# Kernel tuning notes

Hardware: AMD Instinct MI355X
Metric: run time of the kernel (lower is better)

Reference implementation:

```python
import jax, jax.numpy as jnp
import numpy as np

S, B, E, H, Q, T, K, N = 256, 32, 768, 1024, 64, 512, 11, 16
STD = 2.5
EPS = 1e-5


def gaussian_kernel(size, std):
    t = np.linspace(-(size - 1) / 2, (size - 1) / 2, size)
    x, y = np.meshgrid(t, t)
    kern = np.exp(-0.5 * (x ** 2 + y ** 2) / std ** 2)
    return (kern / kern.sum()).astype(np.float32)


def setup_inputs() -> dict:
    key = jax.random.key(0)
    ks = jax.random.split(key, 24)
    s = 0.05
    inp = {
        'sentence_batch': jax.random.normal(ks[0], (S, B, E), jnp.float32),
        # forward LSTM params (torch layout: W_ih (4H,E), W_hh (4H,H), gate order i,f,g,o)
        'Wih_f': jax.random.normal(ks[1], (4 * H, E), jnp.float32) * s,
        'Whh_f': jax.random.normal(ks[2], (4 * H, H), jnp.float32) * s,
        'bih_f': jnp.zeros((4 * H,), jnp.float32),
        'bhh_f': jnp.zeros((4 * H,), jnp.float32),
        # backward LSTM params
        'Wih_b': jax.random.normal(ks[3], (4 * H, E), jnp.float32) * s,
        'Whh_b': jax.random.normal(ks[4], (4 * H, H), jnp.float32) * s,
        'bih_b': jnp.zeros((4 * H,), jnp.float32),
        'bhh_b': jnp.zeros((4 * H,), jnp.float32),
        # layer norms
        'g_in': jnp.ones((E,), jnp.float32), 'be_in': jnp.zeros((E,), jnp.float32),
        'g_fw': jnp.ones((H,), jnp.float32), 'be_fw': jnp.zeros((H,), jnp.float32),
        'g_bk': jnp.ones((H,), jnp.float32), 'be_bk': jnp.zeros((H,), jnp.float32),
        'g_sq': jnp.ones((2 * Q,), jnp.float32), 'be_sq': jnp.zeros((2 * Q,), jnp.float32),
        # squeeze + topic linears (torch layout: W (out,in))
        'Wsq': jax.random.normal(ks[5], (Q, H), jnp.float32) * s,
        'bsq': jnp.zeros((Q,), jnp.float32),
        'Wtop': jax.random.normal(ks[6], (T, 2 * Q), jnp.float32) * s,
        'btop': jnp.zeros((T,), jnp.float32),
        'gauss_kern': jnp.asarray(gaussian_kernel(K, STD)),
    }
    return inp


def layer_norm(x, g, b):
    mu = jnp.mean(x, axis=-1, keepdims=True)
    var = jnp.mean((x - mu) ** 2, axis=-1, keepdims=True)
    return g * (x - mu) * jax.lax.rsqrt(var + EPS) + b


def lstm(x, Wih, Whh, bih, bhh):
    # x: (S, B, E) -> hidden states (S, B, H). torch gate order: i, f, g, o.
    h0 = jnp.zeros((x.shape[1], Whh.shape[1]), x.dtype)
    c0 = jnp.zeros_like(h0)
    xg = jnp.einsum('sbe,ge->sbg', x, Wih) + bih  # precompute input gates

    def step(carry, xt):
        h, c = carry
        gates = xt + h @ Whh.T + bhh
        i, f, g, o = jnp.split(gates, 4, axis=-1)
        c = jax.nn.sigmoid(f) * c + jax.nn.sigmoid(i) * jnp.tanh(g)
        h = jax.nn.sigmoid(o) * jnp.tanh(c)
        return (h, c), h

    _, hs = jax.lax.scan(step, (h0, c0), xg)
    return hs


def batch_pca(e, dim):
    # e: (S, B, F) -> projections (B, S, dim) onto top-dim principal axes
    c = e - jnp.mean(e, axis=0)
    cov = jnp.einsum('sbi,sbj->bij', c, c) / e.shape[0]  # (B, F, F), symmetric
    _, evecs = jnp.linalg.eigh(cov)  # ascending eigenvalues
    top = evecs[:, :, ::-1][:, :, :dim]  # (B, F, dim), descending order
    return jnp.einsum('sbf,bfn->bsn', c, top)


def gauss_smooth(x, kern):
    # x: (B, S, N) smoothed with 2D gaussian, SAME padding
    p = (kern.shape[0] - 1) // 2
    y = jax.lax.conv_general_dilated(
        x[:, None, :, :], kern[None, None, :, :], (1, 1), [(p, p), (p, p)])
    return y[:, 0]


def adj_cos(e):
    # cosine similarity between adjacent sequence positions: (B, S, N) -> (B, S-1)
    a, b = e[:, :-1], e[:, 1:]
    num = jnp.sum(a * b, axis=-1)
    den = jnp.linalg.norm(a, axis=-1) * jnp.linalg.norm(b, axis=-1)
    return num / den


def reference(sentence_batch, Wih_f, Whh_f, bih_f, bhh_f, Wih_b, Whh_b, bih_b, bhh_b,
              g_in, be_in, g_fw, be_fw, g_bk, be_bk, g_sq, be_sq,
              Wsq, bsq, Wtop, btop, gauss_kern):
    x = layer_norm(sentence_batch, g_in, be_in)
    x_f = lstm(x, Wih_f, Whh_f, bih_f, bhh_f)
    x_b = lstm(x[::-1], Wih_b, Whh_b, bih_b, bhh_b)[::-1]
    x_f = layer_norm(x_f, g_fw, be_fw)
    x_b = layer_norm(x_b, g_bk, be_bk)
    x_f = jnp.tanh(jnp.einsum('sbh,qh->sbq', x_f, Wsq) + bsq)
    x_b = jnp.tanh(jnp.einsum('sbh,qh->sbq', x_b, Wsq) + bsq)
    xc = layer_norm(jnp.concatenate((x_f, x_b), axis=-1), g_sq, be_sq)
    topic_preds = jnp.einsum('sbq,tq->sbt', xc, Wtop) + btop

    # segmentation path (no-grad in original)
    e_f = batch_pca(jax.lax.stop_gradient(x_f), N)
    e_b = batch_pca(jax.lax.stop_gradient(x_b), N)
    e_f = gauss_smooth(e_f, gauss_kern)
    e_b = gauss_smooth(e_b, gauss_kern)
    d = jnp.sqrt(adj_cos(e_f) * adj_cos(e_b))  # (B, S-1)
    pos = jnp.argmax(d, axis=1)
    return topic_preds, pos
```

## Files before the change

kernel.cpp:

```cpp
#include <hip/hip_runtime.h>
#include <cstdint>
#include <cstddef>

#define SS   256
#define BB   32
#define EE   768
#define HH   1024
#define QQ   64
#define TTOP 512
#define NPC  16
#define G4   4096
#define TCHUNK 32
#define NBLK 256
#define EPSF 1e-5f

#define OFF_XNT   ((size_t)0)
#define OFF_WHHT  ((size_t)6291456)
#define OFF_CT    ((size_t)14680064)
#define OFF_HBUF  ((size_t)14745600)
#define OFF_CNT   ((size_t)14876672)
#define OFF_XG    ((size_t)14877184)
#define OFF_HS    ((size_t)23265792)
#define OFF_XQ    ((size_t)40043008)
#define OFF_CMAT  ((size_t)0)
#define OFF_COV   ((size_t)1048576)
#define OFF_PG    ((size_t)1310720)
#define OFF_COS   ((size_t)1376256)

#define WLKS 4616
#define LSTM_DYN_LDS 153344

#define AST 65
#define EIG_DYN_LDS 133120

#define EPS32D    5.9604644775390625e-8
#define EPS232D   (EPS32D*EPS32D)
#define SAFMIN32D 1.1754943508222875e-38

__device__ __forceinline__ float sigm(float x){ return 1.0f/(1.0f + expf(-x)); }

__device__ __forceinline__ double wsumd(double v){
  #pragma unroll
  for (int o = 32; o; o >>= 1) v += __shfl_xor(v, o, 64);
  return v;
}
__device__ __forceinline__ double wmaxd(double v){
  #pragma unroll
  for (int o = 32; o; o >>= 1) v = fmax(v, __shfl_xor(v, o, 64));
  return v;
}
__device__ __forceinline__ void dlartg_(double f, double g, double& c, double& s, double& r){
  if (g == 0.0){ c = 1.0; s = 0.0; r = f; }
  else if (f == 0.0){ c = 0.0; s = (g >= 0.0) ? 1.0 : -1.0; r = fabs(g); }
  else {
    double d = sqrt(f*f + g*g);
    c = fabs(f)/d;
    r = copysign(d, f);
    s = g/r;
  }
}
__device__ void dlaev2_(double a, double b, double c,
                        double& rt1, double& rt2, double& cs1, double& sn1){
  double sm = a + c, df = a - c, adf = fabs(df), tb = b + b, ab = fabs(tb);
  double acmx, acmn;
  if (fabs(a) > fabs(c)){ acmx = a; acmn = c; } else { acmx = c; acmn = a; }
  double rt;
  if (adf > ab)      rt = adf*sqrt(1.0 + (ab/adf)*(ab/adf));
  else if (adf < ab) rt = ab*sqrt(1.0 + (adf/ab)*(adf/ab));
  else               rt = ab*sqrt(2.0);
  int sgn1;
  if (sm < 0.0){ rt1 = 0.5*(sm - rt); sgn1 = -1; rt2 = (acmx/rt1)*acmn - (b/rt1)*b; }
  else if (sm > 0.0){ rt1 = 0.5*(sm + rt); sgn1 = 1; rt2 = (acmx/rt1)*acmn - (b/rt1)*b; }
  else { rt1 = 0.5*rt; rt2 = -0.5*rt; sgn1 = 1; }
  double cs; int sgn2;
  if (df >= 0.0){ cs = df + rt; sgn2 = 1; } else { cs = df - rt; sgn2 = -1; }
  double acs = fabs(cs);
  if (acs > ab){ double ct = -tb/cs; sn1 = 1.0/sqrt(1.0+ct*ct); cs1 = ct*sn1; }
  else {
    if (ab == 0.0){ cs1 = 1.0; sn1 = 0.0; }
    else { double tn = -cs/tb; cs1 = 1.0/sqrt(1.0+tn*tn); sn1 = tn*cs1; }
  }
  if (sgn1 == sgn2){ double tn = cs1; cs1 = -sn1; sn1 = tn; }
}

__device__ void dsteqr16_(int base, double* d, double* e, double* z16, int ln,
                          double* tmpd, double* tmpz, int* rk){
  if (ln < 16){
    #pragma unroll
    for (int j = 0; j < 16; j++) z16[ln*17+j] = (ln==j) ? 1.0 : 0.0;
  }
  const int n = 16, nm1 = 15;
  int jtot = 0; const int nmaxit = 480;
  int l1 = 0;
  while (l1 < n){
    if (l1 > 0) e[base+l1-1] = 0.0;
    int m = nm1;
    for (int mm = l1; mm < nm1; mm++){
      double tst = fabs(e[base+mm]);
      if (tst == 0.0){ m = mm; break; }
      if (tst <= (sqrt(fabs(d[base+mm]))*sqrt(fabs(d[base+mm+1])))*EPS32D){
        e[base+mm] = 0.0; m = mm; break;
      }
    }
    int l = l1, lend = m;
    l1 = m + 1;
    if (lend == l) continue;
    if (fabs(d[base+lend]) < fabs(d[base+l])){ int t = l; l = lend; lend = t; }
    if (lend > l){
      for (;;){
        int mm = lend;
        for (int k2 = l; k2 < lend; k2++){
          double tst = e[base+k2]*e[base+k2];
          if (tst <= (EPS232D*fabs(d[base+k2]))*fabs(d[base+k2+1]) + SAFMIN32D){ mm = k2; break; }
        }
        if (mm < lend) e[base+mm] = 0.0;
        double p = d[base+l];
        if (mm == l){ l++; if (l <= lend) continue; break; }
        if (mm == l+1){
          double rt1, rt2, cc, ss;
          dlaev2_(d[base+l], e[base+l], d[base+l+1], rt1, rt2, cc, ss);
          if (ln < 16){
            double x = z16[ln*17+l], y = z16[ln*17+l+1];
            z16[ln*17+l]   = cc*x + ss*y;
            z16[ln*17+l+1] = cc*y - ss*x;
          }
          d[base+l] = rt1; d[base+l+1] = rt2; e[base+l] = 0.0;
          l += 2; if (l <= lend) continue; break;
        }
        if (jtot == nmaxit) break;
        jtot++;
        double g = (d[base+l+1]-p)/(2.0*e[base+l]);
        double r = sqrt(g*g+1.0);
        g = d[base+mm] - p + e[base+l]/(g + copysign(r, g));
        double s2 = 1.0, c2 = 1.0; p = 0.0;
        for (int i = mm-1; i >= l; i--){
          double f = s2*e[base+i], b = c2*e[base+i];
          dlartg_(g, f, c2, s2, r);
          if (i != mm-1) e[base+i+1] = r;
          g = d[base+i+1] - p;
          r = (d[base+i]-g)*s2 + 2.0*c2*b;
          p = s2*r;
          d[base+i+1] = g + p;
          g = c2*r - b;
          if (ln < 16){
            double x = z16[ln*17+i], y = z16[ln*17+i+1];
            z16[ln*17+i]   = c2*x - s2*y;
            z16[ln*17+i+1] = s2*x + c2*y;
          }
        }
        d[base+l] -= p; e[base+l] = g;
      }
    } else {
      for (;;){
        int mm = lend;
        for (int k2 = l; k2 > lend; k2--){
          double tst = e[base+k2-1]*e[base+k2-1];
          if (tst <= (EPS232D*fabs(d[base+k2]))*fabs(d[base+k2-1]) + SAFMIN32D){ mm = k2; break; }
        }
        if (mm > lend) e[base+mm-1] = 0.0;
        double p = d[base+l];
        if (mm == l){ l--; if (l >= lend) continue; break; }
        if (mm == l-1){
          double rt1, rt2, cc, ss;
          dlaev2_(d[base+l-1], e[base+l-1], d[base+l], rt1, rt2, cc, ss);
          if (ln < 16){
            double x = z16[ln*17+l-1], y = z16[ln*17+l];
            z16[ln*17+l-1] = cc*x + ss*y;
            z16[ln*17+l]   = cc*y - ss*x;
          }
          d[base+l-1] = rt1; d[base+l] = rt2; e[base+l-1] = 0.0;
          l -= 2; if (l >= lend) continue; break;
        }
        if (jtot == nmaxit) break;
        jtot++;
        double g = (d[base+l-1]-p)/(2.0*e[base+l-1]);
        double r = sqrt(g*g+1.0);
        g = d[base+mm] - p + e[base+l-1]/(g + copysign(r, g));
        double s2 = 1.0, c2 = 1.0; p = 0.0;
        for (int i = mm; i <= l-1; i++){
          double f = s2*e[base+i], b = c2*e[base+i];
          dlartg_(g, f, c2, s2, r);
          if (i != mm) e[base+i-1] = r;
          g = d[base+i] - p;
          r = (d[base+i+1]-g)*s2 + 2.0*c2*b;
          p = s2*r;
          d[base+i] = g + p;
          g = c2*r - b;
          if (ln < 16){
            double x = z16[ln*17+i], y = z16[ln*17+i+1];
            z16[ln*17+i]   = c2*x + s2*y;
            z16[ln*17+i+1] = c2*y - s2*x;
          }
        }
        d[base+l] -= p; e[base+l-1] = g;
      }
    }
  }
  if (ln < 16){
    double di = d[base+ln]; int r = 0;
    for (int j = 0; j < 16; j++){
      double dj = d[base+j];
      if (dj < di || (dj == di && j < ln)) r++;
    }
    rk[ln] = r;
    tmpd[r] = di;
  }
  if (ln < 16){
    for (int j = 0; j < 16; j++) tmpz[ln*16 + rk[j]] = z16[ln*17 + j];
    for (int j = 0; j < 16; j++) z16[ln*17 + j] = tmpz[ln*16 + j];
    d[base+ln] = tmpd[ln];
  }
}

__device__ void dc_merge1(int base, int n1, int n2, double rho_in, int ln,
    double* s_d, double* Zt, double* Ttp,
    double* md, double* mz, double* dl, double* wz, double* lam, double* zh,
    double* ev, double* su, int* indx, int* sec, int* defl, int* prm){
  const int n = n1 + n2;
  double zv = 0.0;
  if (ln < n){
    if (ln < n1) zv = Zt[(size_t)(base+n1-1)*AST + base + ln];
    else         zv = Zt[(size_t)(base+n1)*AST + base + ln];
    if (rho_in < 0.0 && ln >= n1) zv = -zv;
  }
  zv *= 0.70710678118654752440;
  double mdv = (ln < n) ? s_d[base+ln] : 0.0;
  if (ln < n){ mz[ln] = zv; md[ln] = mdv; }
  double rho = fabs(2.0*rho_in);
  if (ln == 0){
    int i1 = 0, i2 = n1, k = 0;
    while (i1 < n1 && i2 < n){
      if (md[i2] < md[i1]) indx[k++] = i2++; else indx[k++] = i1++;
    }
    while (i1 < n1) indx[k++] = i1++;
    while (i2 < n)  indx[k++] = i2++;
  }
  double dmax = wmaxd((ln<n) ? fabs(mdv) : 0.0);
  double zmax = wmaxd((ln<n) ? fabs(zv) : 0.0);
  double tol = 8.0*EPS32D*fmax(dmax, zmax);
  int K = 0, ndefl = 0, pj = -1;
  for (int j = 0; j < n; j++){
    int nj = indx[j];
    if (rho*fabs(mz[nj]) <= tol){
      defl[ndefl++] = nj;
    } else if (pj < 0){
      pj = nj;
    } else {
      double sG = mz[pj], cG = mz[nj];
      double tau = sqrt(cG*cG + sG*sG);
      double tdf = md[nj] - md[pj];
      double c = cG/tau, s = -sG/tau;
      if (fabs(tdf*c*s) <= tol){
        mz[nj] = tau; mz[pj] = 0.0;
        if (ln < n){
          double x = Zt[(size_t)(base+ln)*AST + base+pj];
          double y = Zt[(size_t)(base+ln)*AST + base+nj];
          Zt[(size_t)(base+ln)*AST + base+pj] = c*x + s*y;
          Zt[(size_t)(base+ln)*AST + base+nj] = c*y - s*x;
        }
        double t2 = md[pj]*c*c + md[nj]*s*s;
        double t3 = md[pj]*s*s + md[nj]*c*c;
        md[nj] = t3; md[pj] = t2;
        defl[ndefl++] = pj;
        pj = nj;
      } else {
        sec[K] = pj; dl[K] = md[pj]; wz[K] = mz[pj]; K++;
        pj = nj;
      }
    }
  }
  if (pj >= 0){ sec[K] = pj; dl[K] = md[pj]; wz[K] = mz[pj]; K++; }
  double wsum2 = wsumd((ln < K) ? wz[ln]*wz[ln] : 0.0);
  if (ln < K){
    double lo = dl[ln];
    double hi = (ln < K-1) ? dl[ln+1] : (dl[K-1] + rho*wsum2);
    for (int it = 0; it < 120; it++){
      double mid = 0.5*(lo+hi);
      if (!(mid > lo) || !(mid < hi)) break;
      double fv = 1.0;
      for (int i2 = 0; i2 < K; i2++) fv += rho*wz[i2]*wz[i2]/(dl[i2]-mid);
      if (fv < 0.0) lo = mid; else hi = mid;
    }
    double lj = 0.5*(lo+hi);
    if (!(lj > dl[ln])) lj = nextafter(dl[ln], 1.0e300);
    lam[ln] = lj;
  }
  if (ln < K){
    double di = dl[ln];
    double prod = lam[K-1] - di;
    for (int j2 = 0; j2 < ln; j2++)   prod *= (lam[j2]-di)/(dl[j2]-di);
    for (int j2 = ln; j2 < K-1; j2++) prod *= (lam[j2]-di)/(dl[j2+1]-di);
    zh[ln] = copysign(sqrt(fabs(prod)), wz[ln]);
  }
  for (int j = 0; j < K; j++){
    double ui = (ln < K) ? zh[ln]/(dl[ln]-lam[j]) : 0.0;
    double nrm = sqrt(wsumd(ui*ui));
    su[ln] = ui/nrm;
    if (ln < n){
      double acc = 0.0;
      for (int i2 = 0; i2 < K; i2++)
        acc += Zt[(size_t)(base+ln)*AST + base + sec[i2]]*su[i2];
      Ttp[(size_t)ln*AST + j] = acc;
    }
    ev[j] = lam[j];
  }
  for (int j = 0; j < ndefl; j++){
    int cj = defl[j];
    if (ln < n) Ttp[(size_t)ln*AST + K + j] = Zt[(size_t)(base+ln)*AST + base + cj];
    ev[K+j] = md[cj];
  }
  if (ln < n){
    double di = ev[ln]; int r = 0;
    for (int j2 = 0; j2 < n; j2++){
      double dj = ev[j2];
      if (dj < di || (dj == di && j2 < ln)) r++;
    }
    prm[r] = ln;
  }
  if (ln < n){
    for (int c2 = 0; c2 < n; c2++)
      Zt[(size_t)(base+ln)*AST + base + c2] = Ttp[(size_t)ln*AST + prm[c2]];
    s_d[base+ln] = ev[prm[ln]];
  }
}

__device__ void dc_merge(int base, int n1, int n2, double rho_in, int tid,
    double* s_d, double* Zt, double* Tt,
    double* md, double* mz, double* dl, double* wz, double* lam, double* zh,
    double* ev, double* su4, int* indx, int* sec, int* defl, int* prm,
    int* sKn){
  const int ln = tid & 63, w = tid >> 6;
  int n = n1 + n2;
  double zv = 0.0;
  if (ln < n){
    if (ln < n1) zv = Zt[(size_t)(base+n1-1)*AST + base + ln];
    else         zv = Zt[(size_t)(base+n1)*AST + base + ln];
    if (rho_in < 0.0 && ln >= n1) zv = -zv;
  }
  zv *= 0.70710678118654752440;
  mz[ln] = (ln < n) ? zv : 0.0;
  md[ln] = (ln < n) ? s_d[base+ln] : 0.0;
  __syncthreads();
  double rho = fabs(2.0*rho_in);
  if (tid == 0){
    int i1 = 0, i2 = n1, k = 0;
    while (i1 < n1 && i2 < n){
      if (md[i2] < md[i1]) indx[k++] = i2++; else indx[k++] = i1++;
    }
    while (i1 < n1) indx[k++] = i1++;
    while (i2 < n)  indx[k++] = i2++;
  }
  __syncthreads();
  double dmax = wmaxd((ln<n) ? fabs(md[ln]) : 0.0);
  double zmax = wmaxd((ln<n) ? fabs(mz[ln]) : 0.0);
  double tol = 8.0*EPS32D*fmax(dmax, zmax);
  if (w == 0){
    int K = 0, ndefl = 0, pj = -1;
    for (int j = 0; j < n; j++){
      int nj = indx[j];
      if (rho*fabs(mz[nj]) <= tol){
        defl[ndefl++] = nj;
      } else if (pj < 0){
        pj = nj;
      } else {
        double sG = mz[pj], cG = mz[nj];
        double tau = sqrt(cG*cG + sG*sG);
        double tdf = md[nj] - md[pj];
        double c = cG/tau, s = -sG/tau;
        if (fabs(tdf*c*s) <= tol){
          mz[nj] = tau; mz[pj] = 0.0;
          if (ln < n){
            double x = Zt[(size_t)(base+ln)*AST + base+pj];
            double y = Zt[(size_t)(base+ln)*AST + base+nj];
            Zt[(size_t)(base+ln)*AST + base+pj] = c*x + s*y;
            Zt[(size_t)(base+ln)*AST + base+nj] = c*y - s*x;
          }
          double t2 = md[pj]*c*c + md[nj]*s*s;
          double t3 = md[pj]*s*s + md[nj]*c*c;
          md[nj] = t3; md[pj] = t2;
          defl[ndefl++] = pj;
          pj = nj;
        } else {
          sec[K] = pj; dl[K] = md[pj]; wz[K] = mz[pj]; K++;
          pj = nj;
        }
      }
    }
    if (pj >= 0){ sec[K] = pj; dl[K] = md[pj]; wz[K] = mz[pj]; K++; }
    if (ln == 0){ sKn[0] = K; sKn[1] = ndefl; }
  }
  __syncthreads();
  const int K = sKn[0], ndefl = sKn[1];
  double wsum2 = wsumd((ln < K) ? wz[ln]*wz[ln] : 0.0);
  {
    bool conv = (ln >= K);
    double lo = 0.0, hi = 0.0;
    if (!conv){
      lo = dl[ln];
      hi = (ln < K-1) ? dl[ln+1] : (dl[K-1] + rho*wsum2);
    }
    const int i2lo = w*16;
    for (int it = 0; it < 120; it++){
      double mid = 0.0;
      if (!conv){
        mid = 0.5*(lo+hi);
        if (!(mid > lo) || !(mid < hi)) conv = true;
      }
      double fp = 0.0;
      if (!conv){
        int i2hi = i2lo + 16; if (i2hi > K) i2hi = K;
        for (int i2 = i2lo; i2 < i2hi; i2++)
          fp += rho*wz[i2]*wz[i2]/(dl[i2]-mid);
      }
      const int p = (it & 1)*256;
      su4[p + w*64 + ln] = fp;
      int alldone = __syncthreads_count(conv ? 1 : 0);
      if (alldone == 256) break;
      if (!conv){
        double fv = 1.0 + su4[p+ln] + su4[p+64+ln] + su4[p+128+ln] + su4[p+192+ln];
        if (fv < 0.0) lo = mid; else hi = mid;
      }
    }
    if (ln < K){
      double lj = 0.5*(lo+hi);
      if (!(lj > dl[ln])) lj = nextafter(dl[ln], 1.0e300);
      lam[ln] = lj;
    }
  }
  __syncthreads();
  if (ln < K){
    double di = dl[ln];
    double prod = lam[K-1] - di;
    for (int j2 = 0; j2 < ln; j2++)   prod *= (lam[j2]-di)/(dl[j2]-di);
    for (int j2 = ln; j2 < K-1; j2++) prod *= (lam[j2]-di)/(dl[j2+1]-di);
    zh[ln] = copysign(sqrt(fabs(prod)), wz[ln]);
  }
  __syncthreads();
  for (int j = w; j < K; j += 4){
    double ui = (ln < K) ? zh[ln]/(dl[ln]-lam[j]) : 0.0;
    double nrm = sqrt(wsumd(ui*ui));
    su4[w*64 + ln] = ui/nrm;
    if (ln < n){
      double acc = 0.0;
      for (int i2 = 0; i2 < K; i2++)
        acc += Zt[(size_t)(base+ln)*AST + base + sec[i2]]*su4[w*64 + i2];
      Tt[(size_t)ln*AST + j] = acc;
    }
    if (ln == 0) ev[j] = lam[j];
  }
  __syncthreads();
  for (int j = 0; j < ndefl; j++){
    int cj = defl[j];
    if (ln < n) Tt[(size_t)ln*AST + K + j] = Zt[(size_t)(base+ln)*AST + base + cj];
    if (ln == 0) ev[K+j] = md[cj];
  }
  __syncthreads();
  if (w == 0 && ln < n){
    double di = ev[ln]; int r = 0;
    for (int j2 = 0; j2 < n; j2++){
      double dj = ev[j2];
      if (dj < di || (dj == di && j2 < ln)) r++;
    }
    prm[r] = ln;
  }
  __syncthreads();
  if (ln < n){
    for (int c2 = 0; c2 < n; c2++)
      Zt[(size_t)(base+ln)*AST + base + c2] = Tt[(size_t)ln*AST + prm[c2]];
  }
  if (ln == 0){ for (int c2 = 0; c2 < n; c2++) s_d[base+c2] = ev[prm[c2]]; }
  __syncthreads();
}

__global__ __launch_bounds__(256) void k_eig(const float* __restrict__ covg,
                                             float* __restrict__ Pg){
  int u = blockIdx.x, tid = threadIdx.x;
  const int ln = tid & 63, w = tid >> 6;
  extern __shared__ double dsm[];
  double* A  = dsm;
  double* Qh = dsm + 4160;
  double* Zt = dsm + 8320;
  double* Tt = dsm + 12480;
  __shared__ double s_d[64], s_e[64], s_tau[64], s_v[64], s_w[64];
  __shared__ double md[64], mz[64], dl[64], wz[64], lam[64], zh[64], ev[64];
  __shared__ double su4[2*4*64];
  __shared__ double z16a[4*272];
  __shared__ int indx[64], sec[64], defl[64], prm[64], sKn[2];

  for (int n = tid; n < 4096; n += 256)
    A[(n >> 6)*AST + (n & 63)] = (double)covg[(size_t)u*4096 + n];
  __syncthreads();

  for (int i = 0; i < 63; i++){
    double alpha = A[(size_t)(i+1)*AST + i];
    double xv = (ln >= i+2) ? A[(size_t)ln*AST + i] : 0.0;
    double xnorm2 = wsumd(xv*xv);
    if (xnorm2 == 0.0){
      if (tid == 0){ s_e[i] = alpha; s_tau[i] = 0.0; }
    } else {
      double beta = -copysign(sqrt(alpha*alpha + xnorm2), alpha);
      double taui = (beta - alpha)/beta;
      double sc = 1.0/(alpha - beta);
      s_v[ln] = (ln == i+1) ? 1.0 : ((ln >= i+2) ? A[(size_t)ln*AST+i]*sc : 0.0);
      __syncthreads();
      if (ln >= i+2) A[(size_t)ln*AST+i] = s_v[ln];
      double wr = 0.0;
      if (ln >= i+1){
        for (int c2 = i+1; c2 < 64; c2++){
          double av = (ln >= c2) ? A[(size_t)ln*AST+c2] : A[(size_t)c2*AST+ln];
          wr += av*s_v[c2];
        }
        wr *= taui;
      }
      double dotwv = wsumd((ln >= i+1) ? wr*s_v[ln] : 0.0);
      double alp2 = -0.5*taui*dotwv;
      wr += alp2*s_v[ln];
      s_w[ln] = (ln >= i+1) ? wr : 0.0;
      __syncthreads();
      if (ln >= i+1){
        for (int c2 = i+1; c2 <= ln; c2++)
          if ((c2 & 3) == w)
            A[(size_t)ln*AST+c2] -= s_v[ln]*s_w[c2] + s_w[ln]*s_v[c2];
      }
      if (tid == 0){ s_e[i] = beta; s_tau[i] = taui; }
    }
    __syncthreads();
  }
  if (w == 0) s_d[ln] = A[(size_t)ln*AST+ln];
  __syncthreads();

  for (int n = tid; n < 4160; n += 256) Qh[n] = 0.0;
  __syncthreads();
  if (w == 0) Qh[(size_t)ln*AST+ln] = 1.0;
  __syncthreads();
  for (int i = 62; i >= 0; i--){
    double taui = s_tau[i];
    if (taui != 0.0){
      s_v[ln] = (ln == i+1) ? 1.0 : ((ln >= i+2) ? A[(size_t)ln*AST+i] : 0.0);
      __syncthreads();
      double dj = 0.0;
      for (int r2 = i+1; r2 < 64; r2++) dj += s_v[r2]*Qh[(size_t)r2*AST+ln];
      dj *= taui;
      for (int r2 = i+1; r2 < 64; r2++)
        if ((r2 & 3) == w)
          Qh[(size_t)r2*AST+ln] -= s_v[r2]*dj;
    }
    __syncthreads();
  }

  double rho_a = s_e[15], rho_b = s_e[47], rho_top = s_e[31];
  if (tid == 0){
    s_d[15] -= fabs(rho_a);   s_d[16] -= fabs(rho_a);
    s_d[31] -= fabs(rho_top); s_d[32] -= fabs(rho_top);
    s_d[47] -= fabs(rho_b);   s_d[48] -= fabs(rho_b);
  }
  for (int n = tid; n < 4160; n += 256) Zt[n] = 0.0;
  __syncthreads();
  dsteqr16_(w*16, s_d, s_e, &z16a[w*272], ln,
            &su4[w*64], Tt + (size_t)w*1040, &indx[w*16]);
  if (ln < 16){
    for (int j = 0; j < 16; j++)
      Zt[(size_t)(w*16+ln)*AST + w*16 + j] = z16a[w*272 + ln*17+j];
  }
  __syncthreads();

  if (w == 0)
    dc_merge1(0, 16, 16, rho_a, ln, s_d, Zt, Tt,
              md, mz, dl, wz, lam, zh, ev, su4,
              indx, sec, defl, prm);
  else if (w == 1)
    dc_merge1(32, 16, 16, rho_b, ln, s_d, Zt, Tt + (size_t)32*AST,
              md+32, mz+32, dl+32, wz+32, lam+32, zh+32, ev+32, su4+64,
              indx+32, sec+32, defl+32, prm+32);
  __syncthreads();

  dc_merge(0, 32, 32, rho_top, tid, s_d, Zt, Tt, md, mz, dl, wz, lam, zh, ev, su4, indx, sec, defl, prm, sKn);

  for (int nn = w; nn < 16; nn += 4){
    double acc = 0.0;
    for (int k = 0; k < 64; k++)
      acc += Qh[(size_t)ln*AST+k]*Zt[(size_t)k*AST + (63-nn)];
    Pg[(size_t)u*1024 + ln*16 + nn] = (float)acc;
  }
}

__global__ void k_ln_in(const float* __restrict__ x, const float* __restrict__ g,
                        const float* __restrict__ be, float* __restrict__ xnT){
  int bid = blockIdx.x; int s = bid >> 5, b = bid & 31;
  int tid = threadIdx.x;
  const float* row = x + ((size_t)(s*BB + b))*EE;
  __shared__ float r1[256], r2[256];
  float su = 0.f, sq = 0.f;
  for (int e = tid; e < EE; e += 256){ float v = row[e]; su += v; sq += v*v; }
  r1[tid] = su; r2[tid] = sq; __syncthreads();
  for (int st = 128; st > 0; st >>= 1){
    if (tid < st){ r1[tid] += r1[tid+st]; r2[tid] += r2[tid+st]; }
    __syncthreads();
  }
  float mu  = r1[0] * (1.0f/EE);
  float var = r2[0] * (1.0f/EE) - mu*mu;
  float rstd = rsqrtf(var + EPSF);
  for (int e = tid; e < EE; e += 256){
    float v = (row[e]-mu)*rstd*g[e] + be[e];
    xnT[((size_t)s*EE + e)*BB + b] = v;
  }
}

__global__ void k_whht(const float* __restrict__ Whh_f, const float* __restrict__ Whh_b,
                       float* __restrict__ WhhT){
  int d  = blockIdx.z;
  const float* Whh = d ? Whh_b : Whh_f;
  int rt = blockIdx.x*32, kt = blockIdx.y*32;
  int tx = threadIdx.x & 31, ty = threadIdx.x >> 5;
  __shared__ float tile[32][33];
  for (int i = ty; i < 32; i += 8)
    tile[i][tx] = Whh[(size_t)(rt+i)*HH + kt+tx];
  __syncthreads();
  for (int i = ty; i < 32; i += 8)
    WhhT[((size_t)d*HH + kt+i)*G4 + rt+tx] = tile[tx][i];
}

__global__ void k_zero(float* __restrict__ p, int n){
  int i = blockIdx.x*blockDim.x + threadIdx.x;
  if (i < n) p[i] = 0.f;
}

__global__ __launch_bounds__(256) void k_xg(const float* __restrict__ xnT,
        const float* __restrict__ Wih_f, const float* __restrict__ Wih_b,
        float* __restrict__ xg, int* __restrict__ cnt, int c){
  if (blockIdx.x == 0 && blockIdx.y == 0 && threadIdx.x < 16)
    __hip_atomic_store(&cnt[threadIdx.x*16], 0, __ATOMIC_RELAXED, __HIP_MEMORY_SCOPE_AGENT);
  int nb = blockIdx.x, rb = blockIdx.y;
  int d = rb >> 5, rloc0 = (rb & 31)*128;
  const float* Wih = d ? Wih_b : Wih_f;
  int tid = threadIdx.x;
  int tx = tid & 15, ty = tid >> 4;
  __shared__ float Al[16*132];
  __shared__ float Bl[16*132];
  float acc[8][8];
  #pragma unroll
  for (int i = 0; i < 8; i++)
    #pragma unroll
    for (int j = 0; j < 8; j++) acc[i][j] = 0.f;
  for (int kc = 0; kc < EE; kc += 16){
    #pragma unroll
    for (int j = 0; j < 8; j++){
      int idx = tid + j*256;
      int n = idx & 127, k = idx >> 7;
      int tglob = c*TCHUNK + nb*4 + (n >> 5);
      int tsrc = d ? (SS-1-tglob) : tglob;
      Al[k*132 + n] = xnT[((size_t)tsrc*EE + kc + k)*BB + (n & 31)];
    }
    #pragma unroll
    for (int j = 0; j < 8; j++){
      int idx = tid + j*256;
      int k = idx & 15, r = idx >> 4;
      Bl[k*132 + r] = Wih[(size_t)(rloc0 + r)*EE + kc + k];
    }
    __syncthreads();
    #pragma unroll
    for (int k = 0; k < 16; k++){
      float4 a0 = *(const float4*)(&Al[k*132 + tx*4]);
      float4 a1 = *(const float4*)(&Al[k*132 + 64 + tx*4]);
      float4 b0 = *(const float4*)(&Bl[k*132 + ty*4]);
      float4 b1 = *(const float4*)(&Bl[k*132 + 64 + ty*4]);
      float av[8] = {a0.x,a0.y,a0.z,a0.w,a1.x,a1.y,a1.z,a1.w};
      float bv[8] = {b0.x,b0.y,b0.z,b0.w,b1.x,b1.y,b1.z,b1.w};
      #pragma unroll
      for (int i = 0; i < 8; i++)
        #pragma unroll
        for (int j2 = 0; j2 < 8; j2++) acc[i][j2] += av[i]*bv[j2];
    }
    __syncthreads();
  }
  #pragma unroll
  for (int j = 0; j < 8; j++){
    int r = rloc0 + ((j < 4) ? (ty*4 + j) : (64 + ty*4 + j - 4));
    #pragma unroll
    for (int ig = 0; ig < 2; ig++){
      int n0 = ig*64 + tx*4;
      int tl = nb*4 + (n0 >> 5), b = n0 & 31;
      float4 o = make_float4(acc[ig*4+0][j], acc[ig*4+1][j], acc[ig*4+2][j], acc[ig*4+3][j]);
      *(float4*)(&xg[(((size_t)tl*8192) + d*G4 + r)*BB + b]) = o;
    }
  }
}

__global__ __launch_bounds__(512) void k_lstm(
    const float* __restrict__ WhhT,
    const float* __restrict__ bih_f, const float* __restrict__ bhh_f,
    const float* __restrict__ bih_b, const float* __restrict__ bhh_b,
    const float* __restrict__ xg, float* __restrict__ hbuf,
    float* __restrict__ cT, float* __restrict__ hs,
    int* __restrict__ cnt, int c)
{
  extern __shared__ float lsm[];
  float* Wl  = lsm;
  float* gl  = lsm + 36928;
  float* cls = lsm + 38080;

  const int blk = blockIdx.x;
  const int d   = blk >> 7;
  const int j0  = (blk & 127) * 8;
  const int tid = threadIdx.x;
  const int ln  = tid & 63;
  const int ksub = ln >> 3;
  const int bg   = ln & 7;
  const int b0   = bg * 4;
  const int cbase = (tid >> 6) * 4;

  const float* bih = d ? bih_b : bih_f;
  const float* bhh = d ? bhh_b : bhh_f;
  const float* WT_d = WhhT + (size_t)d * HH * G4;

  {
    const int cs = tid & 31;
    const int ks = tid >> 5;
    const int g  = cs >> 3, jj = cs & 7;
    const size_t rglob = (size_t)g*HH + j0 + jj;
    for (int kk = 0; kk < 64; kk++){
      int k = kk*16 + ks;
      Wl[(k >> 7)*WLKS + (k & 127)*36 + cs] = WT_d[(size_t)k*G4 + rglob];
    }
  }

  const int pjj = (tid >> 5) & 7, pb = tid & 31;
  float pbias[4];
  if (tid < 256){
    cls[pjj*32 + pb] = cT[((size_t)d*HH + j0 + pjj)*BB + pb];
    #pragma unroll
    for (int g2 = 0; g2 < 4; g2++)
      pbias[g2] = bih[g2*HH + j0 + pjj] + bhh[g2*HH + j0 + pjj];
  }
  __syncthreads();

  for (int tl = 0; tl < TCHUNK; tl++){
    const int s = c*TCHUNK + tl;
    const float* hprev = hbuf + ((size_t)((s & 1)*2 + d))*HH*BB;
    float*       hnext = hbuf + ((size_t)(((s+1) & 1)*2 + d))*HH*BB;

    float xgv[4] = {0.f,0.f,0.f,0.f};
    if (tid < 256){
      const size_t xbase = ((size_t)tl*8192 + (size_t)d*G4)*BB;
      #pragma unroll
      for (int g2 = 0; g2 < 4; g2++)
        xgv[g2] = xg[xbase + (size_t)(g2*HH + j0 + pjj)*BB + pb];
    }

    float acc[4][4];
    #pragma unroll
    for (int i = 0; i < 4; i++)
      #pragma unroll
      for (int j = 0; j < 4; j++) acc[i][j] = 0.f;

    {
      const float* hp = hprev + (size_t)(ksub*128)*BB + b0;
      const float* wrow = &Wl[ksub*WLKS + cbase];
      for (int ib = 0; ib < 128; ib += 16){
        float4 hv[16];
        #pragma unroll
        for (int u = 0; u < 16; u++)
          hv[u] = *(const float4*)(hp + (size_t)(ib+u)*BB);
        #pragma unroll
        for (int u = 0; u < 16; u++){
          float4 wv = *(const float4*)(wrow + (ib+u)*36);
          acc[0][0] += wv.x*hv[u].x; acc[0][1] += wv.x*hv[u].y; acc[0][2] += wv.x*hv[u].z; acc[0][3] += wv.x*hv[u].w;
          acc[1][0] += wv.y*hv[u].x; acc[1][1] += wv.y*hv[u].y; acc[1][2] += wv.y*hv[u].z; acc[1][3] += wv.y*hv[u].w;
          acc[2][0] += wv.z*hv[u].x; acc[2][1] += wv.z*hv[u].y; acc[2][2] += wv.z*hv[u].z; acc[2][3] += wv.z*hv[u].w;
          acc[3][0] += wv.w*hv[u].x; acc[3][1] += wv.w*hv[u].y; acc[3][2] += wv.w*hv[u].z; acc[3][3] += wv.w*hv[u].w;
        }
      }
    }
    #pragma unroll
    for (int i = 0; i < 4; i++)
      #pragma unroll
      for (int j = 0; j < 4; j++){
        float v = acc[i][j];
        v += __shfl_xor(v, 8, 64);
        v += __shfl_xor(v, 16, 64);
        v += __shfl_xor(v, 32, 64);
        acc[i][j] = v;
      }
    if (ksub == 0){
      #pragma unroll
      for (int i = 0; i < 4; i++){
        float4 o = make_float4(acc[i][0], acc[i][1], acc[i][2], acc[i][3]);
        *(float4*)(&gl[(cbase + i)*36 + b0]) = o;
      }
    }
    __syncthreads();
    if (tid < 256){
      float gv[4];
      #pragma unroll
      for (int g2 = 0; g2 < 4; g2++)
        gv[g2] = gl[(g2*8 + pjj)*36 + pb] + pbias[g2] + xgv[g2];
      float iv = sigm(gv[0]), fv = sigm(gv[1]), ggv = tanhf(gv[2]), ov = sigm(gv[3]);
      float cv = fv*cls[pjj*32 + pb] + iv*ggv;
      cls[pjj*32 + pb] = cv;
      float h = ov*tanhf(cv);
      hnext[(size_t)(j0 + pjj)*BB + pb] = h;
      int tsv = d ? (SS-1-s) : s;
      hs[(((size_t)d*SS + tsv)*HH + j0 + pjj)*BB + pb] = h;
    }
    if (tl < TCHUNK-1){
      __syncthreads();
      if (tid == 0){
        __builtin_amdgcn_fence(__ATOMIC_RELEASE, "agent");
        __hip_atomic_fetch_add(&cnt[((blk & 7) + d*8)*16], 1, __ATOMIC_RELAXED, __HIP_MEMORY_SCOPE_AGENT);
        const int target = 16*(tl+1);
        const int lbase = d*8;
        int done = 0;
        while (done < 8){
          done = 0;
          #pragma unroll
          for (int i = 0; i < 8; i++)
            done += (__hip_atomic_load(&cnt[(lbase+i)*16], __ATOMIC_RELAXED, __HIP_MEMORY_SCOPE_AGENT) >= target);
          if (done < 8) __builtin_amdgcn_s_sleep(2);
        }
        __builtin_amdgcn_fence(__ATOMIC_ACQUIRE, "agent");
      }
      __syncthreads();
    }
  }
  __syncthreads();
  if (tid < 256)
    cT[((size_t)d*HH + j0 + pjj)*BB + pb] = cls[pjj*32 + pb];
}

__global__ __launch_bounds__(256) void k_lnproj(const float* __restrict__ hs,
        const float* __restrict__ g_fw, const float* __restrict__ be_fw,
        const float* __restrict__ g_bk, const float* __restrict__ be_bk,
        const float* __restrict__ Wsq, const float* __restrict__ bsq,
        float* __restrict__ xq){
  int t = blockIdx.x, d = blockIdx.y;
  int tid = threadIdx.x;
  const float* gv  = d ? g_bk  : g_fw;
  const float* bev = d ? be_bk : be_fw;
  const float* hrow = hs + ((size_t)d*SS + t)*HH*BB;
  __shared__ float red[256], red2[256];
  __shared__ float smu[32], srs[32];
  __shared__ float ln[32*132];
  __shared__ float wl[64*132];
  {
    int b = tid & 31, jg = tid >> 5;
    float s = 0.f, s2 = 0.f;
    for (int j = jg*128; j < jg*128+128; j++){
      float v = hrow[(size_t)j*BB + b];
      s += v; s2 += v*v;
    }
    red[b*8 + jg] = s; red2[b*8 + jg] = s2; __syncthreads();
    if (tid < 32){
      float a = 0.f, a2 = 0.f;
      for (int k = 0; k < 8; k++){ a += red[tid*8+k]; a2 += red2[tid*8+k]; }
      float mu = a*(1.f/HH), var = a2*(1.f/HH) - mu*mu;
      smu[tid] = mu; srs[tid] = rsqrtf(var + EPSF);
    }
    __syncthreads();
  }
  float acc[4][2] = {{0.f,0.f},{0.f,0.f},{0.f,0.f},{0.f,0.f}};
  int qg = tid & 31, bg = tid >> 5;
  int q0 = qg*2, b0g = bg*4;
  for (int jc = 0; jc < 8; jc++){
    for (int n = tid; n < 4096; n += 256){
      int b = n & 31, jj = n >> 5; int j = jc*128 + jj;
      float v = hrow[(size_t)j*BB + b];
      ln[b*132+jj] = (v - smu[b])*srs[b]*gv[j] + bev[j];
    }
    for (int n = tid; n < 8192; n += 256){
      int q = n >> 7, jj = n & 127;
      wl[q*132+jj] = Wsq[(size_t)q*HH + jc*128 + jj];
    }
    __syncthreads();
    for (int jj = 0; jj < 128; jj += 4){
      float4 w0 = *(const float4*)(&wl[q0*132+jj]);
      float4 w1 = *(const float4*)(&wl[(q0+1)*132+jj]);
      #pragma unroll
      for (int i = 0; i < 4; i++){
        float4 xv = *(const float4*)(&ln[(b0g+i)*132+jj]);
        acc[i][0] += xv.x*w0.x + xv.y*w0.y + xv.z*w0.z + xv.w*w0.w;
        acc[i][1] += xv.x*w1.x + xv.y*w1.y + xv.z*w1.z + xv.w*w1.w;
      }
    }
    __syncthreads();
  }
  #pragma unroll
  for (int i = 0; i < 4; i++)
    #pragma unroll
    for (int u = 0; u < 2; u++){
      float o = tanhf(acc[i][u] + bsq[q0+u]);
      xq[(((size_t)d*SS + t)*BB + (b0g+i))*QQ + q0 + u] = o;
    }
}

__global__ __launch_bounds__(256) void k_topic(const float* __restrict__ xq,
        const float* __restrict__ g_sq, const float* __restrict__ be_sq,
        const float* __restrict__ Wtop, const float* __restrict__ btop,
        float* __restrict__ out){
  int t = blockIdx.x; int tid = threadIdx.x;
  __shared__ float xc[32*132];
  __shared__ float wl[16*520];
  __shared__ float red[256], red2[256];
  __shared__ float smu[32], srs[32];
  for (int n = tid; n < 4096; n += 256){
    int b = n >> 7, q = n & 127;
    float v = (q < 64) ? xq[(((size_t)0*SS + t)*BB + b)*QQ + q]
                       : xq[(((size_t)1*SS + t)*BB + b)*QQ + (q-64)];
    xc[b*132+q] = v;
  }
  __syncthreads();
  {
    int b = tid >> 3, sl = tid & 7;
    float s = 0.f, s2 = 0.f;
    for (int k = 0; k < 16; k++){ float v = xc[b*132 + sl*16 + k]; s += v; s2 += v*v; }
    red[tid] = s; red2[tid] = s2; __syncthreads();
    if (tid < 32){
      float a = 0.f, a2 = 0.f;
      for (int k = 0; k < 8; k++){ a += red[tid*8+k]; a2 += red2[tid*8+k]; }
      float mu = a*(1.f/128.f), var = a2*(1.f/128.f) - mu*mu;
      smu[tid] = mu; srs[tid] = rsqrtf(var + EPSF);
    }
    __syncthreads();
    for (int n = tid; n < 4096; n += 256){
      int b2 = n >> 7, q = n & 127;
      xc[b2*132+q] = (xc[b2*132+q]-smu[b2])*srs[b2]*g_sq[q] + be_sq[q];
    }
    __syncthreads();
  }
  int og = tid & 63, bg = tid >> 6;
  int o0 = og*8, b0 = bg*8;
  float acc[8][8];
  #pragma unroll
  for (int i = 0; i < 8; i++)
    #pragma unroll
    for (int j = 0; j < 8; j++) acc[i][j] = 0.f;
  for (int kc = 0; kc < 128; kc += 16){
    for (int n = tid; n < 8192; n += 256){
      int o = n >> 4, kk = n & 15;
      wl[kk*520 + o] = Wtop[(size_t)o*128 + kc + kk];
    }
    __syncthreads();
    #pragma unroll
    for (int kk = 0; kk < 16; kk++){
      float4 w0 = *(const float4*)(&wl[kk*520+o0]);
      float4 w1 = *(const float4*)(&wl[kk*520+o0+4]);
      float wv[8] = {w0.x,w0.y,w0.z,w0.w,w1.x,w1.y,w1.z,w1.w};
      int k = kc + kk;
      #pragma unroll
      for (int bi = 0; bi < 8; bi++){
        float xv = xc[(b0+bi)*132 + k];
        #pragma unroll
        for (int oi = 0; oi < 8; oi++) acc[bi][oi] += xv*wv[oi];
      }
    }
    __syncthreads();
  }
  #pragma unroll
  for (int bi = 0; bi < 8; bi++){
    int b = b0 + bi;
    #pragma unroll
    for (int oi = 0; oi < 8; oi++)
      out[((size_t)t*BB + b)*TTOP + o0 + oi] = acc[bi][oi] + btop[o0+oi];
  }
}

__global__ __launch_bounds__(256) void k_pca1(const float* __restrict__ xq,
        float* __restrict__ cmat, float* __restrict__ covg){
  int u = blockIdx.x; int d = u >> 5, b = u & 31;
  int tid = threadIdx.x;
  __shared__ float red[256];
  __shared__ float smq[64];
  {
    int q = tid & 63, tg = tid >> 6;
    float s = 0.f;
    for (int t2 = tg*64; t2 < tg*64+64; t2++)
      s += xq[(((size_t)d*SS + t2)*BB + b)*QQ + q];
    red[tid] = s; __syncthreads();
    if (tid < 64) smq[tid] = (red[tid]+red[tid+64]+red[tid+128]+red[tid+192])*(1.f/SS);
    __syncthreads();
  }
  float* cm = cmat + (size_t)u*SS*QQ;
  for (int n = tid; n < SS*QQ; n += 256){
    int t2 = n >> 6, q = n & 63;
    cm[n] = xq[(((size_t)d*SS + t2)*BB + b)*QQ + q] - smq[q];
  }
  __syncthreads();
  {
    int pg = (tid & 15)*4, qg = (tid >> 4)*4;
    float a[4][4] = {{0}};
    for (int t2 = 0; t2 < SS; t2++){
      const float* cr = cm + (size_t)t2*QQ;
      float4 cp = *(const float4*)(cr+pg);
      float4 cq = *(const float4*)(cr+qg);
      float pv[4] = {cp.x,cp.y,cp.z,cp.w}, qv[4] = {cq.x,cq.y,cq.z,cq.w};
      #pragma unroll
      for (int i = 0; i < 4; i++)
        #pragma unroll
        for (int j2 = 0; j2 < 4; j2++) a[i][j2] += pv[i]*qv[j2];
    }
    #pragma unroll
    for (int i = 0; i < 4; i++)
      #pragma unroll
      for (int j2 = 0; j2 < 4; j2++)
        covg[(size_t)u*4096 + (pg+i)*64 + qg+j2] = a[i][j2]*(1.f/SS);
  }
}

__global__ __launch_bounds__(256) void k_pca2(const float* __restrict__ cmat,
        const float* __restrict__ Pg, const float* __restrict__ kern,
        float* __restrict__ cosb){
  int u = blockIdx.x; int tid = threadIdx.x;
  __shared__ float sP[1024];
  __shared__ float sE[4096];
  __shared__ float sY[4096];
  __shared__ float kb[121];
  __shared__ float nn2[256];
  if (tid < 121) kb[tid] = kern[tid];
  for (int n = tid; n < 1024; n += 256) sP[n] = Pg[(size_t)u*1024 + n];
  __syncthreads();
  const float* cm = cmat + (size_t)u*SS*QQ;
  for (int m = tid; m < SS*NPC; m += 256){
    int t2 = m >> 4, n = m & 15;
    const float* cr = cm + (size_t)t2*QQ;
    float acc = 0.f;
    for (int i = 0; i < 64; i++) acc += cr[i]*sP[i*16+n];
    sE[m] = acc;
  }
  __syncthreads();
  for (int m = tid; m < SS*NPC; m += 256){
    int t2 = m >> 4, n = m & 15;
    float acc = 0.f;
    for (int a2 = 0; a2 < 11; a2++){
      int ta = t2 + a2 - 5;
      if (ta < 0 || ta >= SS) continue;
      #pragma unroll
      for (int b2 = 0; b2 < 11; b2++){
        int nb = n + b2 - 5;
        if (nb < 0 || nb >= NPC) continue;
        acc += kb[a2*11+b2]*sE[ta*16+nb];
      }
    }
    sY[m] = acc;
  }
  __syncthreads();
  {
    float acc = 0.f;
    #pragma unroll
    for (int n = 0; n < 16; n++){ float v = sY[tid*16+n]; acc += v*v; }
    nn2[tid] = acc;
  }
  __syncthreads();
  if (tid < 255){
    float num = 0.f;
    #pragma unroll
    for (int n = 0; n < 16; n++) num += sY[tid*16+n]*sY[(tid+1)*16+n];
    cosb[(size_t)u*256 + tid] = num/(sqrtf(nn2[tid])*sqrtf(nn2[tid+1]));
  }
}

__global__ void k_pos(const float* __restrict__ cosb, float* __restrict__ out){
  __shared__ float mx[256];
  __shared__ int   mi[256];
  int tid = threadIdx.x;
  for (int b = 0; b < 32; b++){
    float v = -1e30f;
    if (tid < 255){
      float cf = cosb[(size_t)(b)*256 + tid];
      float cb = cosb[(size_t)(32+b)*256 + tid];
      v = sqrtf(cf*cb);
      if (isnan(v)) v = INFINITY;
    }
    mx[tid] = v; __syncthreads();
    for (int st = 128; st > 0; st >>= 1){
      if (tid < st) mx[tid] = fmaxf(mx[tid], mx[tid+st]);
      __syncthreads();
    }
    float m = mx[0]; __syncthreads();
    mi[tid] = (tid < 255 && v == m) ? tid : (1<<30);
    __syncthreads();
    for (int st = 128; st > 0; st >>= 1){
      if (tid < st) mi[tid] = min(mi[tid], mi[tid+st]);
      __syncthreads();
    }
    if (tid == 0) out[(size_t)SS*BB*TTOP + b] = (float)mi[0];
    __syncthreads();
  }
}

extern "C" void kernel_launch(void* const* d_in, const int* in_sizes, int n_in,
                              void* d_out, int out_size, void* d_ws, size_t ws_size,
                              hipStream_t stream){
  (void)in_sizes; (void)n_in; (void)out_size; (void)ws_size;
  const float* x      = (const float*)d_in[0];
  const float* Wih_f  = (const float*)d_in[1];
  const float* Whh_f  = (const float*)d_in[2];
  const float* bih_f  = (const float*)d_in[3];
  const float* bhh_f  = (const float*)d_in[4];
  const float* Wih_b  = (const float*)d_in[5];
  const float* Whh_b  = (const float*)d_in[6];
  const float* bih_b  = (const float*)d_in[7];
  const float* bhh_b  = (const float*)d_in[8];
  const float* g_in   = (const float*)d_in[9];
  const float* be_in  = (const float*)d_in[10];
  const float* g_fw   = (const float*)d_in[11];
  const float* be_fw  = (const float*)d_in[12];
  const float* g_bk   = (const float*)d_in[13];
  const float* be_bk  = (const float*)d_in[14];
  const float* g_sq   = (const float*)d_in[15];
  const float* be_sq  = (const float*)d_in[16];
  const float* Wsq    = (const float*)d_in[17];
  const float* bsq    = (const float*)d_in[18];
  const float* Wtop   = (const float*)d_in[19];
  const float* btop   = (const float*)d_in[20];
  const float* gkern  = (const float*)d_in[21];

  float* ws    = (float*)d_ws;
  float* xnT   = ws + OFF_XNT;
  float* WhhT  = ws + OFF_WHHT;
  float* cT    = ws + OFF_CT;
  float* hbuf  = ws + OFF_HBUF;
  int*   cnt   = (int*)(ws + OFF_CNT);
  float* xg    = ws + OFF_XG;
  float* hs    = ws + OFF_HS;
  float* xq    = ws + OFF_XQ;
  float* cmat  = ws + OFF_CMAT;
  float* covg  = ws + OFF_COV;
  float* Pg    = ws + OFF_PG;
  float* cosb  = ws + OFF_COS;
  float* out   = (float*)d_out;

  hipFuncSetAttribute((const void*)k_eig,
                      hipFuncAttributeMaxDynamicSharedMemorySize, EIG_DYN_LDS);
  hipFuncSetAttribute((const void*)k_lstm,
                      hipFuncAttributeMaxDynamicSharedMemorySize, LSTM_DYN_LDS);

  k_zero<<<dim3(768), dim3(256), 0, stream>>>(cT, 196608);
  k_ln_in<<<dim3(SS*BB), dim3(256), 0, stream>>>(x, g_in, be_in, xnT);
  k_whht<<<dim3(128, 32, 2), dim3(256), 0, stream>>>(Whh_f, Whh_b, WhhT);
  for (int c = 0; c < SS/TCHUNK; c++){
    k_xg<<<dim3(8, 64), dim3(256), 0, stream>>>(xnT, Wih_f, Wih_b, xg, cnt, c);
    k_lstm<<<dim3(NBLK), dim3(512), LSTM_DYN_LDS, stream>>>(WhhT, bih_f, bhh_f, bih_b, bhh_b,
                                                            xg, hbuf, cT, hs, cnt, c);
  }
  k_lnproj<<<dim3(SS,2), dim3(256), 0, stream>>>(hs, g_fw, be_fw, g_bk, be_bk, Wsq, bsq, xq);
  k_topic<<<dim3(SS), dim3(256), 0, stream>>>(xq, g_sq, be_sq, Wtop, btop, out);
  k_pca1<<<dim3(64), dim3(256), 0, stream>>>(xq, cmat, covg);
  k_eig<<<dim3(64), dim3(256), EIG_DYN_LDS, stream>>>(covg, Pg);
  k_pca2<<<dim3(64), dim3(256), 0, stream>>>(cmat, Pg, gkern, cosb);
  k_pos<<<dim3(1), dim3(256), 0, stream>>>(cosb, out);
}
```

Measured before the change: 7.415 ms.

## Remap LSTM recurrent k-split across waves with LDS tree reduction

Reassigns the recurrent matvec work so each wave owns one 128-wide k slice and each lane owns a gate-column/batch tile, instead of splitting k across lanes within a wave. The cross-k partial sums are now combined through a three-level LDS tree reduction with extra barriers, replacing the intra-wave shuffle reduction. The weight LDS stride drops its padding (36 to 32). Within a wave the hidden-state loads now cover one k row rather than eight, which should cut global traffic per wave. The cost is three extra block-wide syncs per timestep and possible LDS bank conflicts from the unpadded stride.

```diff
diff --git a/kernel.cpp b/kernel.cpp
--- a/kernel.cpp
+++ b/kernel.cpp
@@ -27,8 +27,7 @@
 #define OFF_PG    ((size_t)1310720)
 #define OFF_COS   ((size_t)1376256)
 
-#define WLKS 4616
-#define LSTM_DYN_LDS 153344
+#define LSTM_DYN_LDS 153088
 
 #define AST 65
 #define EIG_DYN_LDS 133120
@@ -696,18 +695,20 @@
 {
   extern __shared__ float lsm[];
   float* Wl  = lsm;
-  float* gl  = lsm + 36928;
-  float* cls = lsm + 38080;
+  float* red = lsm + 32768;
+  float* gl  = lsm + 36864;
+  float* cls = lsm + 38016;
 
   const int blk = blockIdx.x;
   const int d   = blk >> 7;
   const int j0  = (blk & 127) * 8;
   const int tid = threadIdx.x;
   const int ln  = tid & 63;
-  const int ksub = ln >> 3;
-  const int bg   = ln & 7;
-  const int b0   = bg * 4;
-  const int cbase = (tid >> 6) * 4;
+  const int w   = tid >> 6;
+  const int cg  = ln >> 3;
+  const int bg  = ln & 7;
+  const int b0  = bg * 4;
+  const int cbase = cg * 4;
 
   const float* bih = d ? bih_b : bih_f;
   const float* bhh = d ? bhh_b : bhh_f;
@@ -720,7 +721,7 @@
     const size_t rglob = (size_t)g*HH + j0 + jj;
     for (int kk = 0; kk < 64; kk++){
       int k = kk*16 + ks;
-      Wl[(k >> 7)*WLKS + (k & 127)*36 + cs] = WT_d[(size_t)k*G4 + rglob];
+      Wl[(k >> 7)*4096 + (k & 127)*32 + cs] = WT_d[(size_t)k*G4 + rglob];
     }
   }
 
@@ -754,8 +755,8 @@
       for (int j = 0; j < 4; j++) acc[i][j] = 0.f;
 
     {
-      const float* hp = hprev + (size_t)(ksub*128)*BB + b0;
-      const float* wrow = &Wl[ksub*WLKS + cbase];
+      const float* hp = hprev + (size_t)(w*128)*BB + b0;
+      const float* wrow = &Wl[w*4096 + cbase];
       for (int ib = 0; ib < 128; ib += 16){
         float4 hv[16];
         #pragma unroll
@@ -763,7 +764,7 @@
           hv[u] = *(const float4*)(hp + (size_t)(ib+u)*BB);
         #pragma unroll
         for (int u = 0; u < 16; u++){
-          float4 wv = *(const float4*)(wrow + (ib+u)*36);
+          float4 wv = *(const float4*)(wrow + (ib+u)*32);
           acc[0][0] += wv.x*hv[u].x; acc[0][1] += wv.x*hv[u].y; acc[0][2] += wv.x*hv[u].z; acc[0][3] += wv.x*hv[u].w;
           acc[1][0] += wv.y*hv[u].x; acc[1][1] += wv.y*hv[u].y; acc[1][2] += wv.y*hv[u].z; acc[1][3] += wv.y*hv[u].w;
           acc[2][0] += wv.z*hv[u].x; acc[2][1] += wv.z*hv[u].y; acc[2][2] += wv.z*hv[u].z; acc[2][3] += wv.z*hv[u].w;
@@ -771,19 +772,54 @@
         }
       }
     }
-    #pragma unroll
-    for (int i = 0; i < 4; i++)
-      #pragma unroll
-      for (int j = 0; j < 4; j++){
-        float v = acc[i][j];
-        v += __shfl_xor(v, 8, 64);
-        v += __shfl_xor(v, 16, 64);
-        v += __shfl_xor(v, 32, 64);
-        acc[i][j] = v;
-      }
-    if (ksub == 0){
+    if (w >= 4){
+      float* rp = &red[(w-4)*1024];
+      #pragma unroll
+      for (int i = 0; i < 4; i++)
+        #pragma unroll
+        for (int j = 0; j < 4; j++) rp[(i*4+j)*64 + ln] = acc[i][j];
+    }
+    __syncthreads();
+    if (w < 4){
+      const float* rp = &red[w*1024];
+      #pragma unroll
+      for (int i = 0; i < 4; i++)
+        #pragma unroll
+        for (int j = 0; j < 4; j++) acc[i][j] += rp[(i*4+j)*64 + ln];
+    }
+    if (w == 2 || w == 3){
+      float* rp = &red[w*1024];
+      #pragma unroll
+      for (int i = 0; i < 4; i++)
+        #pragma unroll
+        for (int j = 0; j < 4; j++) rp[(i*4+j)*64 + ln] = acc[i][j];
+    }
+    __syncthreads();
+    if (w == 0){
+      const float* rp = &red[2*1024];
+      #pragma unroll
+      for (int i = 0; i < 4; i++)
+        #pragma unroll
+        for (int j = 0; j < 4; j++) acc[i][j] += rp[(i*4+j)*64 + ln];
+    }
+    if (w == 1){
+      const float* rp = &red[3*1024];
+      float* wp = &red[1*1024];
+      #pragma unroll
+      for (int i = 0; i < 4; i++)
+        #pragma unroll
+        for (int j = 0; j < 4; j++){
+          acc[i][j] += rp[(i*4+j)*64 + ln];
+          wp[(i*4+j)*64 + ln] = acc[i][j];
+        }
+    }
+    __syncthreads();
+    if (w == 0){
+      const float* rp = &red[1*1024];
       #pragma unroll
       for (int i = 0; i < 4; i++){
+        #pragma unroll
+        for (int j = 0; j < 4; j++) acc[i][j] += rp[(i*4+j)*64 + ln];
         float4 o = make_float4(acc[i][0], acc[i][1], acc[i][2], acc[i][3]);
         *(float4*)(&gl[(cbase + i)*36 + b0]) = o;
       }
```

New measurement: 7.378 ms. About the same (-0.5%).
